# Kernel tuning notes

Measured on AMD Instinct MI355X. Metric: run time of the kernel, lower is better.

## Reference

```python
import jax, jax.numpy as jnp
import numpy as np

S_DIM = 4096
N_NODES = 4096
N_EDGES = 32768


def _coarsen(ei_np, N):
    """Integer-only greedy coarsening, faithful to MNGRAPH.forward's while-loop.
    Returns (select order, flattened neighbor indices, segment ids, per-hub
    neighbor counts, forward-fill indices replicating the stale-M behavior for
    empty neighborhoods, and the remapped final edge_index)."""
    ei = ei_np.astype(np.int64).copy()
    I = np.bincount(ei[0], minlength=N)
    O = np.bincount(ei[1], minlength=N)
    order = np.argsort(-(I + O), kind='stable')  # torch.argsort(D, descending=True)
    visits = np.zeros(N, dtype=bool)
    select = []
    nbr_idx, nbr_seg, counts = [], [], []
    while order.size > 0:
        node = int(order[0])
        select.append(node)
        visits[node] = True
        # H = unique neighbors of node in the CURRENT (rewritten) edge_index
        H = np.unique(np.concatenate([ei[1][ei[0] == node], ei[0][ei[1] == node]]))
        visits[H] = True
        order = order[~visits[order]]
        # rewrite: endpoints in H that are not already-selected hubs -> node
        Hn = H[~np.isin(H, np.asarray(select, dtype=np.int64))]
        ei[np.isin(ei, Hn)] = node
        ei = ei[:, ei[0] != ei[1]]  # drop self-loops
        # append reversed edges that are not already present (pair-code isin
        # == the original O(E^2) all/any comparison, computed efficiently)
        code = ei[0] * N + ei[1]
        rcode = ei[1] * N + ei[0]
        new = ~np.isin(rcode, code)
        ei = np.concatenate([ei, ei[::-1][:, new]], axis=1)
        k = len(select) - 1
        nbr_idx.append(H)
        nbr_seg.append(np.full(H.shape[0], k, dtype=np.int64))
        counts.append(H.shape[0])
    select = np.asarray(select, dtype=np.int64)
    sort_sel = np.sort(select)
    ei_out = np.searchsorted(sort_sel, ei)  # compact node ids
    counts = np.asarray(counts, dtype=np.int64)
    # forward-fill: when H is empty the original appends the previous (stale) M
    fill = np.arange(select.shape[0])
    for i in range(select.shape[0]):
        if counts[i] == 0:
            fill[i] = fill[i - 1] if i > 0 else 0
    nbr = np.concatenate(nbr_idx) if nbr_idx else np.zeros(0, np.int64)
    seg = np.concatenate(nbr_seg) if nbr_seg else np.zeros(0, np.int64)
    return select, nbr, seg, counts, fill, ei_out


def setup_inputs() -> dict:
    key = jax.random.key(0)
    k1, k2, k3, k4 = jax.random.split(key, 4)
    x = jax.random.normal(k1, (N_NODES, S_DIM), dtype=jnp.float32)
    edge_index = jax.random.randint(k2, (2, N_EDGES), 0, N_NODES, dtype=jnp.int64)
    bound = float(np.sqrt(6.0 / (1.0 + S_DIM)))  # xavier_uniform on (1, S)
    W1 = jax.random.uniform(k3, (S_DIM,), jnp.float32, -bound, bound)
    W2 = jax.random.uniform(k4, (S_DIM,), jnp.float32, -bound, bound)
    B1 = jnp.zeros((S_DIM,), jnp.float32)
    B2 = jnp.zeros((S_DIM,), jnp.float32)
    return {"x": x, "edge_index": edge_index, "W1": W1, "W2": W2, "B1": B1, "B2": B2}


def reference(x, edge_index, W1, W2, B1, B2):
    N = x.shape[0]
    sel, nbr, seg, counts, fill, ei_out = _coarsen(np.asarray(edge_index), N)
    K = sel.shape[0]
    # Dn = x[n]*W1+B1 for every neighbor of every hub; per-hub mean via segment_sum
    Dn = x[jnp.asarray(nbr)] * W1 + B1                      # [T, S]
    sums = jax.ops.segment_sum(Dn, jnp.asarray(seg), num_segments=K)
    denom = jnp.maximum(jnp.asarray(counts), 1).astype(x.dtype)[:, None]
    mean_Dn = sums / denom                                  # [K, S]
    Dv = x[jnp.asarray(sel)] * W2 + B2                      # [K, S]
    END = jnp.concatenate([Dv, mean_Dn], axis=1)            # [K, 2S]
    END = END[jnp.asarray(fill)]                            # stale-M replication
    return END, jnp.asarray(ei_out)
```

## Files before the change

### kernel.cpp

```cpp
#include <hip/hip_runtime.h>
#include <hip/hip_bf16.h>

#define NT 1024
#define NNODES 4096
#define ECAP 65536

__device__ __forceinline__ int blockScanExcl(int v, int* s_w, int* total) {
    const int tid  = threadIdx.x;
    const int lane = tid & 63;
    const int wv   = tid >> 6;
    int x = v;
#pragma unroll
    for (int off = 1; off < 64; off <<= 1) {
        int t = __shfl_up(x, off, 64);
        if (lane >= off) x += t;
    }
    if (lane == 63) s_w[wv] = x;
    __syncthreads();
    if (tid < 16) {
        int y = s_w[tid];
#pragma unroll
        for (int off = 1; off < 16; off <<= 1) {
            int t = __shfl_up(y, off, 16);
            if (tid >= off) y += t;
        }
        s_w[tid] = y;
    }
    __syncthreads();
    int base = wv ? s_w[wv - 1] : 0;
    int tot  = s_w[15];
    __syncthreads();
    *total = tot;
    return base + x - v;
}

__global__ __launch_bounds__(NT, 1)
void phaseA1(const int* __restrict__ ei, int E0,
             int* __restrict__ U, int* __restrict__ V,
             unsigned int* __restrict__ BM,
             int* __restrict__ NBR, int* __restrict__ OTH,
             int* __restrict__ ORDV, int* __restrict__ ROFFG, int* __restrict__ RENDG,
             int* __restrict__ HAND)
{
    __shared__ unsigned short s_order[NNODES];
    __shared__ unsigned char  s_vis[NNODES];
    __shared__ unsigned int   s_hb[NNODES / 32];
    __shared__ int s_roff[NNODES];
    __shared__ int s_rend[NNODES];
    __shared__ int s_tmp[NNODES];
    __shared__ int s_w[16];
    __shared__ int s_bc[16];

    const int tid = threadIdx.x;

    for (int i = tid; i < NNODES; i += NT) { s_vis[i] = 0; s_tmp[i] = 0; }
    for (int i = tid; i < NNODES / 32; i += NT) s_hb[i] = 0;
    if (tid < 16) s_bc[tid] = 0;
    __syncthreads();

    for (int i = tid; i < E0; i += NT)
        if (ei[2 * i + 1] != 0) s_bc[9] = 1;
    __syncthreads();
    const int is64 = !s_bc[9];

    for (int e = tid; e < E0; e += NT) {
        int uu = ei[is64 ? 2 * e : e];
        int vv = ei[is64 ? 2 * (E0 + e) : (E0 + e)];
        U[e] = uu; V[e] = vv;
        atomicAdd(&s_tmp[uu], 1);
        atomicAdd(&s_tmp[vv], 1);
    }
    __syncthreads();
    for (int n = tid; n < NNODES; n += NT) atomicMax(&s_bc[7], s_tmp[n]);
    __syncthreads();
    const int maxd = s_bc[7];

    for (int d = maxd; d >= 0; --d) {
        int n0 = tid * 4;
        int f0 = (s_tmp[n0] == d), f1 = (s_tmp[n0 + 1] == d);
        int f2 = (s_tmp[n0 + 2] == d), f3 = (s_tmp[n0 + 3] == d);
        int tot;
        int off = blockScanExcl(f0 + f1 + f2 + f3, s_w, &tot);
        int idx = s_bc[4] + off;
        if (f0) s_order[idx++] = (unsigned short)n0;
        if (f1) s_order[idx++] = (unsigned short)(n0 + 1);
        if (f2) s_order[idx++] = (unsigned short)(n0 + 2);
        if (f3) s_order[idx++] = (unsigned short)(n0 + 3);
        __syncthreads();
        if (tid == 0) s_bc[4] += tot;
        __syncthreads();
    }

    if (tid == 0) {
        int nd = s_order[0];
        s_bc[0] = nd; s_vis[nd] = 1;
    }
    __syncthreads();
    {
        const int node = s_bc[0];
        for (int e = tid; e < E0; e += NT) {
            int uu = U[e], vv = V[e];
            if (uu == node) {
                int w = vv; unsigned m = 1u << (w & 31);
                unsigned old = atomicOr(&s_hb[w >> 5], m);
                if (!(old & m)) { int i = atomicAdd(&s_bc[2], 1); s_tmp[i] = w; s_vis[w] = 1; }
            }
            if (vv == node) {
                int w = uu; unsigned m = 1u << (w & 31);
                unsigned old = atomicOr(&s_hb[w >> 5], m);
                if (!(old & m)) { int i = atomicAdd(&s_bc[2], 1); s_tmp[i] = w; s_vis[w] = 1; }
            }
        }
        __syncthreads();
        for (int e = tid; e < E0; e += NT) {
            int uu = U[e];
            if (uu != node && ((s_hb[uu >> 5] >> (uu & 31)) & 1)) U[e] = node;
            int vv = V[e];
            if (vv != node && ((s_hb[vv >> 5] >> (vv & 31)) & 1)) V[e] = node;
        }
        __syncthreads();
    }

    for (int i = tid; i < (1 << 19); i += NT) BM[i] = 0u;
    __syncthreads();
    for (int e = tid; e < E0; e += NT) {
        int uu = U[e], vv = V[e];
        if (uu != vv) {
            unsigned code = ((unsigned)uu << 12) | (unsigned)vv;
            atomicOr(&BM[code >> 5], 1u << (code & 31));
        }
    }
    __syncthreads();
    for (int t = 0; t < E0; t += NT) {
        int e = t + tid, flag = 0, uu = 0, vv = 0;
        if (e < E0) {
            uu = U[e]; vv = V[e];
            if (uu != vv) {
                unsigned rc = ((unsigned)vv << 12) | (unsigned)uu;
                unsigned old = atomicOr(&BM[rc >> 5], 0u);
                flag = !((old >> (rc & 31)) & 1u);
            }
        }
        int tot;
        int off = blockScanExcl(flag, s_w, &tot);
        if (flag) { int r = s_bc[5] + off; U[E0 + r] = vv; V[E0 + r] = uu; }
        __syncthreads();
        if (tid == 0) s_bc[5] += tot;
        __syncthreads();
    }
    const int E1 = E0 + s_bc[5];

    for (int n = tid; n < NNODES; n += NT) s_roff[n] = 0;
    __syncthreads();
    for (int e = tid; e < E1; e += NT) {
        int uu = U[e], vv = V[e];
        if (uu != vv) { atomicAdd(&s_roff[uu], 1); atomicAdd(&s_roff[vv], 1); }
    }
    __syncthreads();
    {
        int n0 = tid * 4;
        int c0 = s_roff[n0], c1 = s_roff[n0 + 1], c2 = s_roff[n0 + 2], c3 = s_roff[n0 + 3];
        int tot;
        int off = blockScanExcl(c0 + c1 + c2 + c3, s_w, &tot);
        int st = off;
        s_roff[n0] = st;     s_rend[n0] = st;     st += c0;
        s_roff[n0 + 1] = st; s_rend[n0 + 1] = st; st += c1;
        s_roff[n0 + 2] = st; s_rend[n0 + 2] = st; st += c2;
        s_roff[n0 + 3] = st; s_rend[n0 + 3] = st;
    }
    __syncthreads();
    for (int e = tid; e < E1; e += NT) {
        int uu = U[e], vv = V[e];
        if (uu != vv) {
            int p = atomicAdd(&s_rend[uu], 1);
            int q = atomicAdd(&s_rend[vv], 1);
            OTH[p] = vv; OTH[q] = uu;
        }
    }
    __syncthreads();
    {
        const int cnt0 = s_bc[2];
        for (int i = tid; i < cnt0; i += NT) NBR[i] = s_tmp[i];
    }
    for (int i = tid; i < NNODES; i += NT) {
        int nd = (int)s_order[i];
        ORDV[i]  = nd | (s_vis[nd] ? 0x8000 : 0);
        ROFFG[i] = s_roff[i];
        RENDG[i] = s_rend[i];
    }
    if (tid == 0) { HAND[0] = E1; HAND[1] = s_bc[2]; HAND[2] = s_bc[0]; }
}

__global__ __launch_bounds__(64, 1)
void phaseA2(const int* __restrict__ OTH, int* __restrict__ NBR,
             const int* __restrict__ ORDV, const int* __restrict__ ROFFG,
             const int* __restrict__ RENDG, const int* __restrict__ HAND,
             int* __restrict__ SEL, int* __restrict__ CNTS,
             int* __restrict__ NST, int* __restrict__ FIL, int* __restrict__ SC,
             int* __restrict__ LABG, int* __restrict__ RNKG)
{
    __shared__ unsigned short s_ordvis[NNODES];
    __shared__ unsigned short s_pos[NNODES];
    __shared__ unsigned short s_lab[NNODES];
    __shared__ unsigned short s_so[NNODES];
    __shared__ int s_cnt[NNODES];
    __shared__ int s_stamp[NNODES];
    __shared__ int s_roff[NNODES];
    __shared__ int s_rend[NNODES];
    __shared__ unsigned char s_sel[NNODES];
    __shared__ int s_nc[1];

    const int ln = threadIdx.x;
    const unsigned long long ltm = (1ull << ln) - 1ull;
    const int cnt0 = HAND[1], hub0 = HAND[2];

    for (int i = ln; i < NNODES; i += 64) {
        int ov = ORDV[i];
        s_ordvis[i] = (unsigned short)ov;
        s_pos[ov & 0x7FFF] = (unsigned short)i;
        s_roff[i] = ROFFG[i];
        s_rend[i] = RENDG[i];
        s_lab[i] = (unsigned short)i;
        s_stamp[i] = 0; s_sel[i] = 0; s_cnt[i] = 0;
    }
    if (ln == 0) {
        s_sel[hub0] = 1; s_so[0] = (unsigned short)hub0;
        s_cnt[0] = cnt0; s_nc[0] = cnt0;
    }

    int p = 0, k = 1;
    for (;;) {
        int node = -1;
        while (p < NNODES) {
            int idx = p + ln;
            int ov = (idx < NNODES) ? (int)s_ordvis[idx] : 0x8000;
            unsigned long long bal = __ballot(!(ov & 0x8000));
            if (bal != 0ull) {
                int sl = __ffsll((long long)bal) - 1;
                node = __shfl(ov, sl, 64) & 0x7FFF;
                p += sl + 1;
                break;
            }
            p += 64;
        }
        if (node < 0) break;
        if (ln == 0) { s_sel[node] = 1; s_so[k] = (unsigned short)node; }
        const int rb = s_roff[node], re = s_rend[node];
        const int begin = s_nc[0];
        for (int s0 = rb; s0 < re; s0 += 128) {
            int sA = s0 + ln, sB = s0 + 64 + ln;
            int oA = (sA < re) ? OTH[sA] : -1;
            int oB = (sB < re) ? OTH[sB] : -1;
            if (oA >= 0) {
                int w = (int)s_lab[oA];
                if (w != node) {
                    int old = atomicMax(&s_stamp[w], k);
                    if (old < k) {
                        int i = atomicAdd(&s_nc[0], 1);
                        NBR[i] = w;
                        s_ordvis[s_pos[w]] = (unsigned short)(0x8000 | w);
                        if (!s_sel[w]) s_lab[w] = (unsigned short)node;
                    }
                }
            }
            if (oB >= 0) {
                int w = (int)s_lab[oB];
                if (w != node) {
                    int old = atomicMax(&s_stamp[w], k);
                    if (old < k) {
                        int i = atomicAdd(&s_nc[0], 1);
                        NBR[i] = w;
                        s_ordvis[s_pos[w]] = (unsigned short)(0x8000 | w);
                        if (!s_sel[w]) s_lab[w] = (unsigned short)node;
                    }
                }
            }
        }
        if (ln == 0) s_cnt[k] = s_nc[0] - begin;
        k++;
    }
    const int K = k;

    {
        int base = 0;
        for (int c = 0; c < NNODES / 64; ++c) {
            int n = c * 64 + ln;
            int f = s_sel[n];
            unsigned long long b = __ballot(f);
            s_stamp[n] = base + __popcll(b & ltm);
            base += __popcll(b);
        }
    }
    {
        int nb = 0;
        for (int c = 0; c * 64 < K; ++c) {
            int i = c * 64 + ln;
            int cv = (i < K) ? s_cnt[i] : 0;
            int x = cv;
#pragma unroll
            for (int off = 1; off < 64; off <<= 1) {
                int t = __shfl_up(x, off, 64);
                if (ln >= off) x += t;
            }
            if (i < K) { NST[i] = nb + x - cv; CNTS[i] = cv; SEL[i] = (int)s_so[i]; }
            nb += __shfl(x, 63, 64);
        }
    }
    {
        int carry = 0;
        for (int c = 0; c * 64 < K; ++c) {
            int i = c * 64 + ln;
            int f = (i < K) && (s_cnt[i] > 0);
            unsigned long long b = __ballot(f);
            unsigned long long m = b & ((ln == 63) ? ~0ull : ((1ull << (ln + 1)) - 1ull));
            int fil = m ? (c * 64 + 63 - __clzll(m)) : carry;
            if (i < K) FIL[i] = fil;
            carry = b ? (c * 64 + 63 - __clzll(b)) : carry;
        }
    }
    if (ln == 0) SC[0] = K;
    for (int i = ln; i < NNODES; i += 64) {
        LABG[i] = (int)s_lab[i];
        RNKG[i] = s_stamp[i];
    }
}

__global__ __launch_bounds__(NT, 1)
void phaseA3(const int* __restrict__ U, const int* __restrict__ V,
             const int* __restrict__ LABG, const int* __restrict__ RNKG,
             const int* __restrict__ HAND, int* __restrict__ SC,
             int* __restrict__ TMP, float* __restrict__ out)
{
    __shared__ unsigned short l_lab[NNODES];
    __shared__ int l_rnk[NNODES];
    __shared__ int s_w[16];
    __shared__ int s_base[1];

    const int tid = threadIdx.x;
    for (int i = tid; i < NNODES; i += NT) {
        l_lab[i] = (unsigned short)LABG[i];
        l_rnk[i] = RNKG[i];
    }
    if (tid == 0) s_base[0] = 0;
    __syncthreads();

    const int E1 = HAND[0];
    const int K  = SC[0];
    const size_t obase = (size_t)K * 8192;

    for (int t = 0; t < E1; t += NT) {
        int e = t + tid, flag = 0, ru = 0, rv = 0;
        if (e < E1) {
            int uu = (int)l_lab[U[e]], vv = (int)l_lab[V[e]];
            if (uu != vv) { flag = 1; ru = l_rnk[uu]; rv = l_rnk[vv]; }
        }
        int tot;
        int off = blockScanExcl(flag, s_w, &tot);
        if (flag) {
            int r = s_base[0] + off;
            out[obase + (size_t)r] = (float)ru;
            TMP[r] = rv;
        }
        __syncthreads();
        if (tid == 0) s_base[0] += tot;
        __syncthreads();
    }
    const int Ef = s_base[0];
    if (tid == 0) SC[1] = Ef;
    for (int r = tid; r < Ef; r += NT)
        out[obase + (size_t)Ef + (size_t)r] = (float)TMP[r];
}

__global__ __launch_bounds__(256, 4)
void phaseB(const float* __restrict__ x,
            const float* __restrict__ W1, const float* __restrict__ W2,
            const float* __restrict__ B1, const float* __restrict__ B2,
            const int* __restrict__ NBR, const int* __restrict__ SEL,
            const int* __restrict__ CNTS, const int* __restrict__ NST,
            const int* __restrict__ FIL, const int* __restrict__ SC,
            float* __restrict__ out)
{
    const int K = SC[0];
    const int k = blockIdx.x;
    if (k >= K) return;
    const int kk   = FIL[k];
    const int node = SEL[kk];
    const int cnt  = CNTS[kk];
    const int st   = NST[kk];
    const int tid  = threadIdx.x;
    const float4* x4 = (const float4*)x;

    float4 acc[4];
#pragma unroll
    for (int j = 0; j < 4; j++) acc[j] = make_float4(0.f, 0.f, 0.f, 0.f);

    for (int r = 0; r < cnt; ++r) {
        const float4* row = x4 + (size_t)NBR[st + r] * 1024;
#pragma unroll
        for (int j = 0; j < 4; j++) {
            float4 t = row[tid + j * 256];
            acc[j].x += t.x; acc[j].y += t.y; acc[j].z += t.z; acc[j].w += t.w;
        }
    }

    const float fc  = (float)cnt;
    const float inv = 1.0f / (float)(cnt > 1 ? cnt : 1);
    const float4* xr = x4 + (size_t)node * 1024;
    float4* o4 = (float4*)(out + (size_t)k * 8192);

#pragma unroll
    for (int j = 0; j < 4; j++) {
        int c = tid + j * 256;
        float4 w1 = ((const float4*)W1)[c], b1 = ((const float4*)B1)[c];
        float4 w2 = ((const float4*)W2)[c], b2 = ((const float4*)B2)[c];
        float4 xv = xr[c];
        float4 pd, pm;
        pd.x = xv.x * w2.x + b2.x;
        pd.y = xv.y * w2.y + b2.y;
        pd.z = xv.z * w2.z + b2.z;
        pd.w = xv.w * w2.w + b2.w;
        pm.x = (acc[j].x * w1.x + fc * b1.x) * inv;
        pm.y = (acc[j].y * w1.y + fc * b1.y) * inv;
        pm.z = (acc[j].z * w1.z + fc * b1.z) * inv;
        pm.w = (acc[j].w * w1.w + fc * b1.w) * inv;
        o4[c] = pd;
        o4[1024 + c] = pm;
    }
}

extern "C" void kernel_launch(void* const* d_in, const int* in_sizes, int n_in,
                              void* d_out, int out_size, void* d_ws, size_t ws_size,
                              hipStream_t stream)
{
    const float* x  = (const float*)d_in[0];
    const int*   ei = (const int*)d_in[1];
    const float* W1 = (const float*)d_in[2];
    const float* W2 = (const float*)d_in[3];
    const float* B1 = (const float*)d_in[4];
    const float* B2 = (const float*)d_in[5];
    const int E0 = in_sizes[1] / 2;

    char* w = (char*)d_ws;
    int* U = (int*)w;
    int* V = U + ECAP;
    unsigned int* BM = (unsigned int*)(V + ECAP);
    int* OTH = (int*)BM;
    int* NBR = OTH + 2 * ECAP;
    int* TMP = NBR + 2 * ECAP;
    char* meta = (char*)BM + (2u << 20);
    int* SEL   = (int*)meta;
    int* CNTS  = SEL  + NNODES;
    int* NST   = CNTS + NNODES;
    int* FIL   = NST  + NNODES;
    int* SC    = FIL  + NNODES;
    int* ORDV  = SC   + 16;
    int* ROFFG = ORDV + NNODES;
    int* RENDG = ROFFG + NNODES;
    int* LABG  = RENDG + NNODES;
    int* RNKG  = LABG + NNODES;
    int* HAND  = RNKG + NNODES;
    float* out = (float*)d_out;

    hipLaunchKernelGGL(phaseA1, dim3(1), dim3(NT), 0, stream,
                       ei, E0, U, V, BM, NBR, OTH, ORDV, ROFFG, RENDG, HAND);
    hipLaunchKernelGGL(phaseA2, dim3(1), dim3(64), 0, stream,
                       OTH, NBR, ORDV, ROFFG, RENDG, HAND,
                       SEL, CNTS, NST, FIL, SC, LABG, RNKG);
    hipLaunchKernelGGL(phaseA3, dim3(1), dim3(NT), 0, stream,
                       U, V, LABG, RNKG, HAND, SC, TMP, out);
    hipLaunchKernelGGL(phaseB, dim3(NNODES), dim3(256), 0, stream,
                       x, W1, W2, B1, B2, NBR, SEL, CNTS, NST, FIL, SC, out);
}
```

Before: 968.2 us.

## Parallelize serial coarsening phases: counting-sort order, batched scans, prefetched hub scan

```diff
diff --git a/kernel.cpp b/kernel.cpp
--- a/kernel.cpp
+++ b/kernel.cpp
@@ -4,6 +4,11 @@
 #define NT 1024
 #define NNODES 4096
 #define ECAP 65536
+
+__global__ __launch_bounds__(256)
+void zeroBM(int4* __restrict__ bm) {
+    bm[(size_t)blockIdx.x * 256 + threadIdx.x] = make_int4(0, 0, 0, 0);
+}
 
 __device__ __forceinline__ int blockScanExcl(int v, int* s_w, int* total) {
     const int tid  = threadIdx.x;
@@ -44,10 +49,12 @@
 {
     __shared__ unsigned short s_order[NNODES];
     __shared__ unsigned char  s_vis[NNODES];
+    __shared__ unsigned char  s_rank[NNODES];
     __shared__ unsigned int   s_hb[NNODES / 32];
     __shared__ int s_roff[NNODES];
     __shared__ int s_rend[NNODES];
     __shared__ int s_tmp[NNODES];
+    __shared__ int s_mat[64][65];
     __shared__ int s_w[16];
     __shared__ int s_bc[16];
 
@@ -75,20 +82,61 @@
     __syncthreads();
     const int maxd = s_bc[7];
 
-    for (int d = maxd; d >= 0; --d) {
-        int n0 = tid * 4;
-        int f0 = (s_tmp[n0] == d), f1 = (s_tmp[n0 + 1] == d);
-        int f2 = (s_tmp[n0 + 2] == d), f3 = (s_tmp[n0 + 3] == d);
-        int tot;
-        int off = blockScanExcl(f0 + f1 + f2 + f3, s_w, &tot);
-        int idx = s_bc[4] + off;
-        if (f0) s_order[idx++] = (unsigned short)n0;
-        if (f1) s_order[idx++] = (unsigned short)(n0 + 1);
-        if (f2) s_order[idx++] = (unsigned short)(n0 + 2);
-        if (f3) s_order[idx++] = (unsigned short)(n0 + 3);
-        __syncthreads();
-        if (tid == 0) s_bc[4] += tot;
-        __syncthreads();
+    if (maxd < 64) {
+        const int wv = tid >> 6, lane = tid & 63;
+        const unsigned long long ltm = (1ull << lane) - 1ull;
+        for (int g = wv; g < 64; g += 16) {
+            int n = g * 64 + lane;
+            int d = s_tmp[n];
+            int rk = 0;
+            for (int dd = 0; dd < 64; ++dd) {
+                unsigned long long bal = __ballot(d == dd);
+                if (lane == 0) s_mat[dd][g] = __popcll(bal);
+                if (d == dd) rk = __popcll(bal & ltm);
+            }
+            s_rank[n] = (unsigned char)rk;
+        }
+        __syncthreads();
+        if (tid < 64) {
+            int run = 0;
+            for (int g = 0; g < 64; ++g) { int t = s_mat[tid][g]; s_mat[tid][g] = run; run += t; }
+            s_mat[tid][64] = run;
+        }
+        __syncthreads();
+        if (tid < 64) {
+            int x = s_mat[tid][64];
+#pragma unroll
+            for (int off = 1; off < 64; off <<= 1) {
+                int t = __shfl_up(x, off, 64);
+                if (tid >= off) x += t;
+            }
+            int T = __shfl(x, 63, 64);
+            s_mat[tid][64] = T - x;
+        }
+        __syncthreads();
+        for (int g = wv; g < 64; g += 16) {
+            int n = g * 64 + lane;
+            int d = s_tmp[n];
+            int pos = s_mat[d][64] + s_mat[d][g] + (int)s_rank[n];
+            s_order[pos] = (unsigned short)n;
+        }
+        __syncthreads();
+    } else {
+        for (int d = maxd; d >= 0; --d) {
+            int n0 = tid * 4;
+            int f0 = (s_tmp[n0] == d), f1 = (s_tmp[n0 + 1] == d);
+            int f2 = (s_tmp[n0 + 2] == d), f3 = (s_tmp[n0 + 3] == d);
+            int tot;
+            int off = blockScanExcl(f0 + f1 + f2 + f3, s_w, &tot);
+            int idx = s_bc[4] + off;
+            if (f0) s_order[idx++] = (unsigned short)n0;
+            if (f1) s_order[idx++] = (unsigned short)(n0 + 1);
+            if (f2) s_order[idx++] = (unsigned short)(n0 + 2);
+            if (f3) s_order[idx++] = (unsigned short)(n0 + 3);
+            __syncthreads();
+            if (tid == 0) s_bc[4] += tot;
+            __syncthreads();
+        }
     }
 
     if (tid == 0) {
@@ -121,8 +169,6 @@
         __syncthreads();
     }
 
-    for (int i = tid; i < (1 << 19); i += NT) BM[i] = 0u;
-    __syncthreads();
     for (int e = tid; e < E0; e += NT) {
         int uu = U[e], vv = V[e];
         if (uu != vv) {
@@ -131,19 +177,30 @@
         }
     }
     __syncthreads();
-    for (int t = 0; t < E0; t += NT) {
-        int e = t + tid, flag = 0, uu = 0, vv = 0;
-        if (e < E0) {
-            uu = U[e]; vv = V[e];
-            if (uu != vv) {
-                unsigned rc = ((unsigned)vv << 12) | (unsigned)uu;
-                unsigned old = atomicOr(&BM[rc >> 5], 0u);
-                flag = !((old >> (rc & 31)) & 1u);
+    for (int t0 = 0; t0 < E0; t0 += NT * 32) {
+        unsigned fm = 0u;
+        const int base = t0 + tid * 32;
+        for (int j = 0; j < 32; ++j) {
+            int e = base + j;
+            if (e < E0) {
+                int uu = U[e], vv = V[e];
+                if (uu != vv) {
+                    unsigned rc = ((unsigned)vv << 12) | (unsigned)uu;
+                    unsigned old = atomicOr(&BM[rc >> 5], 0u);
+                    if (!((old >> (rc & 31)) & 1u)) fm |= (1u << j);
+                }
             }
         }
         int tot;
-        int off = blockScanExcl(flag, s_w, &tot);
-        if (flag) { int r = s_bc[5] + off; U[E0 + r] = vv; V[E0 + r] = uu; }
+        int off = blockScanExcl(__popc(fm), s_w, &tot);
+        int r = s_bc[5] + off;
+        unsigned m = fm;
+        while (m) {
+            int j = __ffs((int)m) - 1; m &= m - 1;
+            int e = base + j;
+            U[E0 + r] = V[e]; V[E0 + r] = U[e];
+            ++r;
+        }
         __syncthreads();
         if (tid == 0) s_bc[5] += tot;
         __syncthreads();
@@ -154,7 +211,7 @@
     __syncthreads();
     for (int e = tid; e < E1; e += NT) {
         int uu = U[e], vv = V[e];
-        if (uu != vv) { atomicAdd(&s_roff[uu], 1); atomicAdd(&s_roff[vv], 1); }
+        if (uu != vv) atomicAdd(&s_roff[uu], 1);
     }
     __syncthreads();
     {
@@ -173,8 +230,7 @@
         int uu = U[e], vv = V[e];
         if (uu != vv) {
             int p = atomicAdd(&s_rend[uu], 1);
-            int q = atomicAdd(&s_rend[vv], 1);
-            OTH[p] = vv; OTH[q] = uu;
+            OTH[p] = vv;
         }
     }
     __syncthreads();
@@ -208,7 +264,6 @@
     __shared__ int s_roff[NNODES];
     __shared__ int s_rend[NNODES];
     __shared__ unsigned char s_sel[NNODES];
-    __shared__ int s_nc[1];
 
     const int ln = threadIdx.x;
     const unsigned long long ltm = (1ull << ln) - 1ull;
@@ -225,10 +280,13 @@
     }
     if (ln == 0) {
         s_sel[hub0] = 1; s_so[0] = (unsigned short)hub0;
-        s_cnt[0] = cnt0; s_nc[0] = cnt0;
-    }
-
+        s_cnt[0] = cnt0;
+    }
+
+    int nc = cnt0;
     int p = 0, k = 1;
+    int pf_node = -1, pf_rb = 0, pf_re = 0, pf_val = -1;
+
     for (;;) {
         int node = -1;
         while (p < NNODES) {
@@ -245,38 +303,58 @@
         }
         if (node < 0) break;
         if (ln == 0) { s_sel[node] = 1; s_so[k] = (unsigned short)node; }
-        const int rb = s_roff[node], re = s_rend[node];
-        const int begin = s_nc[0];
-        for (int s0 = rb; s0 < re; s0 += 128) {
-            int sA = s0 + ln, sB = s0 + 64 + ln;
-            int oA = (sA < re) ? OTH[sA] : -1;
-            int oB = (sB < re) ? OTH[sB] : -1;
-            if (oA >= 0) {
-                int w = (int)s_lab[oA];
-                if (w != node) {
-                    int old = atomicMax(&s_stamp[w], k);
-                    if (old < k) {
-                        int i = atomicAdd(&s_nc[0], 1);
-                        NBR[i] = w;
-                        s_ordvis[s_pos[w]] = (unsigned short)(0x8000 | w);
-                        if (!s_sel[w]) s_lab[w] = (unsigned short)node;
-                    }
+
+        int rb, re, v0;
+        if (node == pf_node) { rb = pf_rb; re = pf_re; v0 = pf_val; }
+        else {
+            rb = s_roff[node]; re = s_rend[node];
+            v0 = (rb + ln < re) ? OTH[rb + ln] : -1;
+        }
+
+        {
+            int q = p, cand = -1, cidx = NNODES;
+            while (q < NNODES) {
+                int idx = q + ln;
+                int ov = (idx < NNODES) ? (int)s_ordvis[idx] : 0x8000;
+                unsigned long long bal = __ballot(!(ov & 0x8000));
+                if (bal != 0ull) {
+                    int sl = __ffsll((long long)bal) - 1;
+                    cand = __shfl(ov, sl, 64) & 0x7FFF;
+                    cidx = q + sl;
+                    break;
                 }
-            }
-            if (oB >= 0) {
-                int w = (int)s_lab[oB];
-                if (w != node) {
-                    int old = atomicMax(&s_stamp[w], k);
-                    if (old < k) {
-                        int i = atomicAdd(&s_nc[0], 1);
-                        NBR[i] = w;
-                        s_ordvis[s_pos[w]] = (unsigned short)(0x8000 | w);
-                        if (!s_sel[w]) s_lab[w] = (unsigned short)node;
-                    }
-                }
-            }
-        }
-        if (ln == 0) s_cnt[k] = s_nc[0] - begin;
+                q += 64;
+            }
+            p = (cand >= 0) ? cidx : NNODES;
+            pf_node = cand;
+            if (cand >= 0) {
+                pf_rb = s_roff[cand]; pf_re = s_rend[cand];
+                pf_val = (pf_rb + ln < pf_re) ? OTH[pf_rb + ln] : -1;
+            } else pf_val = -1;
+        }
+
+        const int begin = nc;
+        auto proc = [&](int o) {
+            int w = (o >= 0) ? (int)s_lab[o] : node;
+            bool cnd = (w != node);
+            int old = k;
+            if (cnd) old = atomicMax(&s_stamp[w], k);
+            bool nw = cnd && (old < k);
+            unsigned long long bal = __ballot(nw);
+            if (nw) {
+                int pre = __popcll(bal & ltm);
+                NBR[nc + pre] = w;
+                s_ordvis[s_pos[w]] = (unsigned short)(0x8000 | w);
+                if (!s_sel[w]) s_lab[w] = (unsigned short)node;
+            }
+            nc += __popcll(bal);
+        };
+        proc(v0);
+        for (int s0 = rb + 64; s0 < re; s0 += 64) {
+            int o = (s0 + ln < re) ? OTH[s0 + ln] : -1;
+            proc(o);
+        }
+        if (ln == 0) s_cnt[k] = nc - begin;
         k++;
     }
     const int K = k;
@@ -348,18 +426,39 @@
     const int K  = SC[0];
     const size_t obase = (size_t)K * 8192;
 
-    for (int t = 0; t < E1; t += NT) {
-        int e = t + tid, flag = 0, ru = 0, rv = 0;
-        if (e < E1) {
-            int uu = (int)l_lab[U[e]], vv = (int)l_lab[V[e]];
-            if (uu != vv) { flag = 1; ru = l_rnk[uu]; rv = l_rnk[vv]; }
+    for (int t0 = 0; t0 < E1; t0 += NT * 64) {
+        unsigned long long fm = 0ull;
+        const int base = t0 + tid * 64;
+        if (base + 64 <= E1) {
+            const int4* U4 = (const int4*)(U + base);
+            const int4* V4 = (const int4*)(V + base);
+#pragma unroll
+            for (int q = 0; q < 16; ++q) {
+                int4 a = U4[q], b = V4[q];
+                int j = q * 4;
+                if ((int)l_lab[a.x] != (int)l_lab[b.x]) fm |= 1ull << j;
+                if ((int)l_lab[a.y] != (int)l_lab[b.y]) fm |= 1ull << (j + 1);
+                if ((int)l_lab[a.z] != (int)l_lab[b.z]) fm |= 1ull << (j + 2);
+                if ((int)l_lab[a.w] != (int)l_lab[b.w]) fm |= 1ull << (j + 3);
+            }
+        } else {
+            for (int j = 0; j < 64; ++j) {
+                int e = base + j;
+                if (e < E1) {
+                    if ((int)l_lab[U[e]] != (int)l_lab[V[e]]) fm |= 1ull << j;
+                }
+            }
         }
         int tot;
-        int off = blockScanExcl(flag, s_w, &tot);
-        if (flag) {
-            int r = s_base[0] + off;
-            out[obase + (size_t)r] = (float)ru;
-            TMP[r] = rv;
+        int off = blockScanExcl(__popcll(fm), s_w, &tot);
+        int r = s_base[0] + off;
+        unsigned long long m = fm;
+        while (m) {
+            int j = __ffsll((long long)m) - 1; m &= m - 1;
+            int e = base + j;
+            out[obase + (size_t)r] = (float)l_rnk[(int)l_lab[U[e]]];
+            TMP[r] = l_rnk[(int)l_lab[V[e]]];
+            ++r;
         }
         __syncthreads();
         if (tid == 0) s_base[0] += tot;
@@ -461,6 +560,8 @@
     int* HAND  = RNKG + NNODES;
     float* out = (float*)d_out;
 
+    hipLaunchKernelGGL(zeroBM, dim3(512), dim3(256), 0, stream, (int4*)BM);
+
     hipLaunchKernelGGL(phaseA1, dim3(1), dim3(NT), 0, stream,
                        ei, E0, U, V, BM, NBR, OTH, ORDV, ROFFG, RENDG, HAND);
     hipLaunchKernelGGL(phaseA2, dim3(1), dim3(64), 0, stream,
```

New measurement: 1.190 ms. +22.9%, slower.
